# Performance work log

Hardware: AMD Instinct MI355X
Metric: run time of the kernel (lower is better)

## Reference

```python
import jax, jax.numpy as jnp
import numpy as np

K = 16  # neighbors


def _knn_indices(coords, k):
    # coords: (B, 3, N) -> indices (B, N, k) of k nearest points (incl. self)
    sq = jnp.sum(coords * coords, axis=1)                      # (B, N)
    d2 = sq[:, :, None] + sq[:, None, :] - 2.0 * jnp.einsum('bcn,bcm->bnm', coords, coords)
    _, idx = jax.lax.top_k(-d2, k)                             # smallest distances
    return idx


def _gather(points, idx):
    # points: (B, C, N), idx: (B, N, k) -> (B, C, N, k)
    return jax.vmap(lambda p, i: p[:, i])(points, idx)


def setup_inputs() -> dict:
    key = jax.random.key(0)
    ks = jax.random.split(key, 8)
    B, N, C_IN, C_OUT = 4, 8192, 64, 64
    s = 0.05
    return {
        'features': jax.random.normal(ks[0], (B, C_IN, N), dtype=jnp.float32),
        'coords': jax.random.normal(ks[1], (B, 3, N), dtype=jnp.float32),
        'w_lin': jax.random.normal(ks[2], (3 * C_OUT, C_IN), dtype=jnp.float32) * s,
        'w_theta1': jax.random.normal(ks[3], (C_OUT, 3), dtype=jnp.float32) * s,
        'w_theta2': jax.random.normal(ks[4], (C_OUT, C_OUT), dtype=jnp.float32) * s,
        'w_gamma1': jax.random.normal(ks[5], (C_OUT, C_OUT), dtype=jnp.float32) * s,
        'w_gamma2': jax.random.normal(ks[6], (C_OUT, C_OUT), dtype=jnp.float32) * s,
    }


def reference(features, coords, w_lin, w_theta1, w_theta2, w_gamma1, w_gamma2):
    # KNN (int indices, non-differentiable)
    idx = _knn_indices(coords, K)                              # (B, N, k)

    knn_coords = _gather(coords, idx)                          # (B, 3, N, k)
    rel = coords[:, :, :, None] - knn_coords                   # localize * -1
    delta = jnp.einsum('oc,bcnk->bonk', w_theta1, rel)
    delta = jax.nn.relu(jnp.einsum('oc,bcnk->bonk', w_theta2, delta))  # (B, Co, N, k)

    # input linear -> phi, psi, alpha
    feat3 = jnp.einsum('oc,bcn->bon', w_lin, features)         # (B, 3*Co, N)
    phi, psi, alpha = jnp.split(feat3, 3, axis=1)

    psi_g = _gather(psi, idx)                                  # (B, Co, N, k)
    inputs_gamma = phi[:, :, :, None] - psi_g + delta          # localize*-1 + delta
    g = jnp.einsum('oc,bcnk->bonk', w_gamma1, inputs_gamma)
    g = jax.nn.relu(jnp.einsum('oc,bcnk->bonk', w_gamma2, g))
    rho = jax.nn.softmax(g, axis=-1)                           # softmax over k

    alpha_g = _gather(alpha, idx) + delta                      # (B, Co, N, k)
    return jnp.sum(rho * alpha_g, axis=-1)                     # (B, Co, N)
```

## Files before the change

### kernel.cpp

```cpp
#include <hip/hip_runtime.h>
#include <cstdint>


#define NPT 8192
typedef unsigned long long u64;
typedef unsigned int u32;
typedef unsigned short u16;
typedef __attribute__((ext_vector_type(8))) short bf8_t;
typedef __attribute__((ext_vector_type(4))) float f32x4;

__device__ __forceinline__ u16 f2bf(float x) {
  return (u16)((__float_as_uint(x) + 0x8000u) >> 16);
}
__device__ __forceinline__ u32 pkbf(float lo, float hi) {
  return (u32)f2bf(lo) | ((u32)f2bf(hi) << 16);
}
__device__ __forceinline__ float bf2f(u16 v) {
  return __uint_as_float((u32)v << 16);
}
__device__ __forceinline__ u32 med3u(u32 a, u32 b, u32 c) {
  u32 d;
  asm("v_med3_u32 %0, %1, %2, %3" : "=v"(d) : "v"(a), "v"(b), "v"(c));
  return d;
}
__device__ __forceinline__ u32 wave_min_u32(u32 v) {
  u32 t;
  t = (u32)__builtin_amdgcn_update_dpp((int)v, (int)v, 0x111, 0xF, 0xF, false); v = min(v, t);
  t = (u32)__builtin_amdgcn_update_dpp((int)v, (int)v, 0x112, 0xF, 0xF, false); v = min(v, t);
  t = (u32)__builtin_amdgcn_update_dpp((int)v, (int)v, 0x114, 0xF, 0xF, false); v = min(v, t);
  t = (u32)__builtin_amdgcn_update_dpp((int)v, (int)v, 0x118, 0xF, 0xF, false); v = min(v, t);
  t = (u32)__builtin_amdgcn_update_dpp((int)v, (int)v, 0x142, 0xF, 0xF, false); v = min(v, t);
  t = (u32)__builtin_amdgcn_update_dpp((int)v, (int)v, 0x143, 0xF, 0xF, false); v = min(v, t);
  return (u32)__builtin_amdgcn_readlane((int)v, 63);
}

__global__ __launch_bounds__(256) void fold1_k(
    const float* __restrict__ wg1, const float* __restrict__ wg2,
    const float* __restrict__ wt1, const float* __restrict__ wt2,
    float* __restrict__ G, float* __restrict__ Mrow, float* __restrict__ McT) {
  int t = blockIdx.x * 256 + threadIdx.x;
  if (t < 4096) {
    int o = t >> 6, c = t & 63;
    float acc = 0.f;
    for (int cp = 0; cp < 64; ++cp) acc = fmaf(wg2[o * 64 + cp], wg1[cp * 64 + c], acc);
    G[o * 64 + c] = acc;
  } else if (t < 4096 + 192) {
    int i = t - 4096;
    int o = i / 3, j = i - o * 3;
    float acc = 0.f;
    for (int c = 0; c < 64; ++c) acc = fmaf(wt2[o * 64 + c], wt1[c * 3 + j], acc);
    Mrow[o * 3 + j] = acc;
    McT[j * 64 + o] = acc;
  }
}

__global__ __launch_bounds__(256) void fold2_k(
    const float* __restrict__ G, const float* __restrict__ wl,
    u16* __restrict__ GF, u16* __restrict__ WF) {
  int t = blockIdx.x * 256 + threadIdx.x;
  if (t < 12288) {
    int o = t >> 6, c = t & 63;
    float acc = 0.f;
    if (o < 64) {
      for (int cp = 0; cp < 64; ++cp) acc = fmaf(G[o * 64 + cp], wl[cp * 64 + c], acc);
    } else if (o < 128) {
      for (int cp = 0; cp < 64; ++cp) acc = fmaf(G[(o - 64) * 64 + cp], wl[(64 + cp) * 64 + c], acc);
    } else {
      acc = wl[o * 64 + c];
    }
    int ot = o >> 4, m = o & 15;
    int kh = c >> 5, q = (c >> 3) & 3, j = c & 7;
    WF[(((ot * 2 + kh) * 64) + (q * 16 + m)) * 8 + j] = f2bf(acc);
  } else {
    int i = t - 12288;
    int o = i >> 6, c = i & 63;
    int ot = o >> 4, m = o & 15;
    int kh = c >> 5, q = (c >> 3) & 3, j = c & 7;
    GF[(((ot * 2 + kh) * 64) + (q * 16 + m)) * 8 + j] = f2bf(G[o * 64 + c]);
  }
}

__global__ __launch_bounds__(256) void pack_k(const float* __restrict__ coords,
                                              float4* __restrict__ pack) {
  int g = blockIdx.x * 256 + threadIdx.x;
  int b = g >> 13, n = g & (NPT - 1);
  const float* c = coords + (size_t)b * 3 * NPT;
  float x = c[n], y = c[NPT + n], z = c[2 * NPT + n];
  float sq = __fadd_rn(__fadd_rn(__fmul_rn(x, x), __fmul_rn(y, y)), __fmul_rn(z, z));
  pack[g] = make_float4(x, y, z, sq);
}

#define QPB 8
#define CHUNK 1024
#define NQ 32768
__global__ __launch_bounds__(512) void knn_k(const float4* __restrict__ pack,
                                             u32* __restrict__ part, int qbase) {
  __shared__ float4 C[CHUNK];
  int tid = threadIdx.x;
  int w = tid >> 6, lane = tid & 63;
  int query = qbase + blockIdx.x * QPB + w;
  int b = query >> 13, n = query & (NPT - 1);
  const float4* pk = pack + (size_t)b * NPT;
  float4 q = pk[n];
  float qsq = q.w;
  u32 arr[8];
#pragma unroll
  for (int j = 0; j < 8; ++j) arr[j] = 0xFFFFFFFFu;
  for (int c0 = 0; c0 < NPT; c0 += CHUNK) {
    C[tid] = pk[c0 + tid];
    C[tid + 512] = pk[c0 + tid + 512];
    __syncthreads();
#pragma unroll 4
    for (int t = 0; t < CHUNK / 64; ++t) {
      float4 c4 = C[t * 64 + lane];
      float dot = fmaf(q.z, c4.z, fmaf(q.y, c4.y, q.x * c4.x));
      float d2 = fmaxf(fmaf(-2.f, dot, qsq + c4.w), 0.f);
      u32 key = (__float_as_uint(d2) & 0xFFFFE000u) | (u32)(c0 + t * 64 + lane);
      if (key < arr[7]) {
        arr[7] = med3u(key, arr[6], arr[7]);
        arr[6] = med3u(key, arr[5], arr[6]);
        arr[5] = med3u(key, arr[4], arr[5]);
        arr[4] = med3u(key, arr[3], arr[4]);
        arr[3] = med3u(key, arr[2], arr[3]);
        arr[2] = med3u(key, arr[1], arr[2]);
        arr[1] = med3u(key, arr[0], arr[1]);
        arr[0] = min(arr[0], key);
      }
    }
    __syncthreads();
  }
  u32 mg = 0xFFFFFFFFu;
#pragma unroll 1
  for (int r = 0; r < 24; ++r) {
    u32 m = wave_min_u32(arr[0]);
    if (lane == r) mg = m;
    if (arr[0] == m) {
      arr[0] = arr[1]; arr[1] = arr[2]; arr[2] = arr[3]; arr[3] = arr[4];
      arr[4] = arr[5]; arr[5] = arr[6]; arr[6] = arr[7]; arr[7] = 0xFFFFFFFFu;
    }
  }
  if (lane < 24) part[(size_t)lane * NQ + query] = mg;
}

__global__ __launch_bounds__(64) void refine_k(const float4* __restrict__ pack,
                                               const u32* __restrict__ part,
                                               int* __restrict__ idxk) {
  int g = blockIdx.x * 64 + threadIdx.x;
  int b = g >> 13;
  const float4* pk = pack + (size_t)b * NPT;
  float4 q = pk[g & (NPT - 1)];
  float qx = q.x, qy = q.y, qz = q.z, qs = q.w;
  float bd[16];
  int bi[16];
#pragma unroll
  for (int j = 0; j < 16; ++j) { bd[j] = 1e30f; bi[j] = 0x7FFFFFFF; }
#pragma unroll 4
  for (int j = 0; j < 24; ++j) {
    int m = (int)(part[(size_t)j * NQ + g] & 0x1FFFu);
    float4 pm = pk[m];
    float dot = __fadd_rn(__fadd_rn(__fmul_rn(qx, pm.x), __fmul_rn(qy, pm.y)),
                          __fmul_rn(qz, pm.z));
    float kd = __fsub_rn(__fadd_rn(qs, pm.w), __fmul_rn(2.0f, dot));
    int ki = m;
    if (kd < bd[15] || (kd == bd[15] && ki < bi[15])) {
#pragma unroll
      for (int qq = 0; qq < 16; ++qq) {
        bool cs = (kd < bd[qq]) || (kd == bd[qq] && ki < bi[qq]);
        float td = bd[qq];
        int ti = bi[qq];
        bd[qq] = cs ? kd : td;
        bi[qq] = cs ? ki : ti;
        kd = cs ? td : kd;
        ki = cs ? ti : ki;
      }
    }
  }
#pragma unroll
  for (int j = 0; j < 16; ++j) idxk[(size_t)g * 16 + j] = bi[j];
}

__global__ __launch_bounds__(256) void feat_k(const float* __restrict__ features,
                                              const u16* __restrict__ WF,
                                              float* __restrict__ featA,
                                              u16* __restrict__ featB) {
  int tid = threadIdx.x;
  int w = tid >> 6, l = tid & 63;
  int quad = l >> 4, col = l & 15;
  int P = blockIdx.x * 64 + w * 16 + col;
  int b = P >> 13, n = P & (NPT - 1);
  const float* fb = features + (size_t)b * 64 * NPT + n;
  const bf8_t* wfr = (const bf8_t*)WF;
  bf8_t Bf[2];
#pragma unroll
  for (int kh = 0; kh < 2; ++kh) {
    union { u32 wv[4]; bf8_t v; } ub;
#pragma unroll
    for (int j2 = 0; j2 < 4; ++j2) {
      float lo = fb[(size_t)(kh * 32 + quad * 8 + j2 * 2) * NPT];
      float hi = fb[(size_t)(kh * 32 + quad * 8 + j2 * 2 + 1) * NPT];
      ub.wv[j2] = pkbf(lo, hi);
    }
    Bf[kh] = ub.v;
  }
#pragma unroll
  for (int ot = 0; ot < 12; ++ot) {
    bf8_t A0 = wfr[(ot * 2 + 0) * 64 + l];
    bf8_t A1 = wfr[(ot * 2 + 1) * 64 + l];
    f32x4 acc = {0.f, 0.f, 0.f, 0.f};
    acc = __builtin_amdgcn_mfma_f32_16x16x32_bf16(A0, Bf[0], acc, 0, 0, 0);
    acc = __builtin_amdgcn_mfma_f32_16x16x32_bf16(A1, Bf[1], acc, 0, 0, 0);
    int gr = ot * 16 + quad * 4;
    if (ot < 4) {
      *(float4*)(featA + (size_t)P * 64 + gr) = make_float4(acc[0], acc[1], acc[2], acc[3]);
    } else {
      uint2 wv2 = make_uint2(pkbf(acc[0], acc[1]), pkbf(acc[2], acc[3]));
      *(uint2*)(featB + (size_t)P * 128 + (gr - 64)) = wv2;
    }
  }
}

#define SROW 68
__global__ __launch_bounds__(64) void attn_k(
    const float4* __restrict__ pack, const int* __restrict__ idxk,
    const float* __restrict__ featA, const u16* __restrict__ featB,
    const u16* __restrict__ GF, const float* __restrict__ Mrow,
    const float* __restrict__ McT, float* __restrict__ out) {
  __shared__ u16 S16[64 * SROW];
  int l = threadIdx.x;
  int quad = l >> 4, col = l & 15;
  int Pb = blockIdx.x * 4;
  int b = Pb >> 13;
  int nb0 = Pb & (NPT - 1);
  const float4* pkb = pack + (size_t)b * NPT;
  int idxv = idxk[(size_t)Pb * 16 + l];
  int mve[4];
#pragma unroll
  for (int t = 0; t < 4; ++t) mve[t] = __shfl(idxv, t * 16 + col);
  float relx[4], rely[4], relz[4];
#pragma unroll
  for (int t = 0; t < 4; ++t) {
    float4 own = pkb[nb0 + t];
    float4 nbr = pkb[mve[t]];
    relx[t] = own.x - nbr.x; rely[t] = own.y - nbr.y; relz[t] = own.z - nbr.z;
  }
  bf8_t Bf[4][2];
#pragma unroll
  for (int kh = 0; kh < 2; ++kh) {
    const float* mr = Mrow + (kh * 32 + quad * 8) * 3;
    float m_[24];
#pragma unroll
    for (int i6 = 0; i6 < 6; ++i6) {
      float4 v = *(const float4*)(mr + i6 * 4);
      m_[i6 * 4] = v.x; m_[i6 * 4 + 1] = v.y; m_[i6 * 4 + 2] = v.z; m_[i6 * 4 + 3] = v.w;
    }
#pragma unroll
    for (int t = 0; t < 4; ++t) {
      float u_[8];
#pragma unroll
      for (int j = 0; j < 8; ++j)
        u_[j] = fmaxf(fmaf(m_[j * 3 + 2], relz[t],
                           fmaf(m_[j * 3 + 1], rely[t], m_[j * 3] * relx[t])), 0.f);
      union { u32 w[4]; bf8_t v; } ub;
#pragma unroll
      for (int j2 = 0; j2 < 4; ++j2) ub.w[j2] = pkbf(u_[j2 * 2], u_[j2 * 2 + 1]);
      Bf[t][kh] = ub.v;
    }
  }
  const bf8_t* gfr = (const bf8_t*)GF;
#pragma unroll
  for (int ot = 0; ot < 4; ++ot) {
    bf8_t A0 = gfr[(ot * 2 + 0) * 64 + l];
    bf8_t A1 = gfr[(ot * 2 + 1) * 64 + l];
#pragma unroll
    for (int pt = 0; pt < 4; ++pt) {
      f32x4 acc = {0.f, 0.f, 0.f, 0.f};
      acc = __builtin_amdgcn_mfma_f32_16x16x32_bf16(A0, Bf[pt][0], acc, 0, 0, 0);
      acc = __builtin_amdgcn_mfma_f32_16x16x32_bf16(A1, Bf[pt][1], acc, 0, 0, 0);
      const float* phn = featA + (size_t)(Pb + pt) * 64 + ot * 16 + quad * 4;
      float4 ph = *(const float4*)phn;
      uint2 psw = *(const uint2*)(featB + ((size_t)b * NPT + mve[pt]) * 128 + ot * 16 + quad * 4);
      float g0 = fmaxf(acc[0] + ph.x - bf2f((u16)(psw.x & 0xFFFF)), 0.f);
      float g1 = fmaxf(acc[1] + ph.y - bf2f((u16)(psw.x >> 16)), 0.f);
      float g2 = fmaxf(acc[2] + ph.z - bf2f((u16)(psw.y & 0xFFFF)), 0.f);
      float g3 = fmaxf(acc[3] + ph.w - bf2f((u16)(psw.y >> 16)), 0.f);
      uint2 wv = make_uint2(pkbf(g0, g1), pkbf(g2, g3));
      *(uint2*)&S16[(pt * 16 + col) * SROW + ot * 16 + quad * 4] = wv;
    }
  }
  __syncthreads();
  float mc0 = McT[l], mc1 = McT[64 + l], mc2 = McT[128 + l];
  float accv[4];
#pragma unroll 1
  for (int pj = 0; pj < 4; ++pj) {
    float4 ownq = pkb[nb0 + pj];
    float gvv[16];
    float mx = -1e30f;
#pragma unroll
    for (int r = 0; r < 16; ++r) {
      gvv[r] = bf2f(S16[(pj * 16 + r) * SROW + l]);
      mx = fmaxf(mx, gvv[r]);
    }
    float s = 0.f;
#pragma unroll
    for (int r = 0; r < 16; ++r) {
      float e = __expf(gvv[r] - mx);
      gvv[r] = e;
      s += e;
    }
    float inv = 1.0f / s;
    float acc = 0.f;
#pragma unroll
    for (int r = 0; r < 16; ++r) {
      int si = __builtin_amdgcn_readlane(idxv, pj * 16 + r);
      float4 nbq = pkb[si];
      float dl = fmaxf(fmaf(mc2, ownq.z - nbq.z,
                            fmaf(mc1, ownq.y - nbq.y, mc0 * (ownq.x - nbq.x))), 0.f);
      float al = bf2f(featB[((size_t)b * NPT + si) * 128 + 64 + l]);
      acc = fmaf(gvv[r] * inv, al + dl, acc);
    }
    accv[pj] = acc;
  }
  *(float4*)(out + ((size_t)b * 64 + l) * NPT + nb0) =
      make_float4(accv[0], accv[1], accv[2], accv[3]);
}

extern "C" void kernel_launch(void* const* d_in, const int* in_sizes, int n_in,
                              void* d_out, int out_size, void* d_ws, size_t ws_size,
                              hipStream_t stream) {
  const float* features = (const float*)d_in[0];
  const float* coords = (const float*)d_in[1];
  const float* w_lin = (const float*)d_in[2];
  const float* w_t1 = (const float*)d_in[3];
  const float* w_t2 = (const float*)d_in[4];
  const float* w_g1 = (const float*)d_in[5];
  const float* w_g2 = (const float*)d_in[6];
  float* out = (float*)d_out;
  char* ws = (char*)d_ws;
  float4* pack = (float4*)ws;
  float* G = (float*)(ws + 524288);
  float* Mrow = (float*)(ws + 540672);
  float* McT = (float*)(ws + 541440);
  int* idxk = (int*)(ws + 591360);
  float* featA = (float*)(ws + 2688512);
  u16* featB = (u16*)(ws + 11077120);
  u32* part = (u32*)(ws + 2688512);
  u16* GF = (u16*)(ws + 19465728);
  u16* WF = (u16*)(ws + 19473920);

  fold1_k<<<17, 256, 0, stream>>>(w_g1, w_g2, w_t1, w_t2, G, Mrow, McT);
  fold2_k<<<64, 256, 0, stream>>>(G, w_lin, GF, WF);
  pack_k<<<128, 256, 0, stream>>>(coords, pack);
  knn_k<<<1024, 512, 0, stream>>>(pack, part, 0);
  knn_k<<<1024, 512, 0, stream>>>(pack, part, 8192);
  knn_k<<<1024, 512, 0, stream>>>(pack, part, 16384);
  knn_k<<<1024, 512, 0, stream>>>(pack, part, 24576);
  refine_k<<<512, 64, 0, stream>>>(pack, part, idxk);
  feat_k<<<512, 256, 0, stream>>>(features, WF, featA, featB);
  attn_k<<<8192, 64, 0, stream>>>(pack, idxk, featA, featB, GF, Mrow, McT, out);
}
```

Before: 307.2 us.

## Double-buffer KNN candidate chunks with async LDS loads and prune by wave threshold

The KNN kernel now stages candidate chunks into a double-buffered LDS array using global_load_lds. The next chunk is prefetched while the current one is scanned, and the barrier before the scan is dropped. After each chunk it computes a wave-wide threshold: the maximum over lanes of each lane's best key. Later candidates above that threshold skip the sorted-insert sequence, which is safe because at least 64 better keys already exist. The four per-batch launches are merged into one grid of 4096 blocks. This doubles LDS use per block, which may reduce occupancy, and correctness depends on the async copies finishing before the barrier.

```diff
diff --git a/kernel.cpp b/kernel.cpp
--- a/kernel.cpp
+++ b/kernel.cpp
@@ -32,6 +32,21 @@
   t = (u32)__builtin_amdgcn_update_dpp((int)v, (int)v, 0x142, 0xF, 0xF, false); v = min(v, t);
   t = (u32)__builtin_amdgcn_update_dpp((int)v, (int)v, 0x143, 0xF, 0xF, false); v = min(v, t);
   return (u32)__builtin_amdgcn_readlane((int)v, 63);
+}
+__device__ __forceinline__ u32 wave_max_u32(u32 v) {
+  u32 t;
+  t = (u32)__builtin_amdgcn_update_dpp((int)v, (int)v, 0x111, 0xF, 0xF, false); v = max(v, t);
+  t = (u32)__builtin_amdgcn_update_dpp((int)v, (int)v, 0x112, 0xF, 0xF, false); v = max(v, t);
+  t = (u32)__builtin_amdgcn_update_dpp((int)v, (int)v, 0x114, 0xF, 0xF, false); v = max(v, t);
+  t = (u32)__builtin_amdgcn_update_dpp((int)v, (int)v, 0x118, 0xF, 0xF, false); v = max(v, t);
+  t = (u32)__builtin_amdgcn_update_dpp((int)v, (int)v, 0x142, 0xF, 0xF, false); v = max(v, t);
+  t = (u32)__builtin_amdgcn_update_dpp((int)v, (int)v, 0x143, 0xF, 0xF, false); v = max(v, t);
+  return (u32)__builtin_amdgcn_readlane((int)v, 63);
+}
+__device__ __forceinline__ void lds_cp16(float4* lds_dst, const float4* gsrc) {
+  __builtin_amdgcn_global_load_lds(
+      (const __attribute__((address_space(1))) unsigned int*)(const void*)gsrc,
+      (__attribute__((address_space(3))) unsigned int*)(void*)lds_dst, 16, 0, 0);
 }
 
 __global__ __launch_bounds__(256) void fold1_k(
@@ -94,11 +109,11 @@
 #define CHUNK 1024
 #define NQ 32768
 __global__ __launch_bounds__(512) void knn_k(const float4* __restrict__ pack,
-                                             u32* __restrict__ part, int qbase) {
-  __shared__ float4 C[CHUNK];
+                                             u32* __restrict__ part) {
+  __shared__ float4 C[2][CHUNK];
   int tid = threadIdx.x;
   int w = tid >> 6, lane = tid & 63;
-  int query = qbase + blockIdx.x * QPB + w;
+  int query = blockIdx.x * QPB + w;
   int b = query >> 13, n = query & (NPT - 1);
   const float4* pk = pack + (size_t)b * NPT;
   float4 q = pk[n];
@@ -106,17 +121,23 @@
   u32 arr[8];
 #pragma unroll
   for (int j = 0; j < 8; ++j) arr[j] = 0xFFFFFFFFu;
+  lds_cp16(&C[0][tid], pk + tid);
+  lds_cp16(&C[0][512 + tid], pk + 512 + tid);
+  __syncthreads();
+  u32 tau = 0xFFFFFFFFu;
   for (int c0 = 0; c0 < NPT; c0 += CHUNK) {
-    C[tid] = pk[c0 + tid];
-    C[tid + 512] = pk[c0 + tid + 512];
-    __syncthreads();
+    int cur = (c0 >> 10) & 1;
+    if (c0 + CHUNK < NPT) {
+      lds_cp16(&C[cur ^ 1][tid], pk + (c0 + CHUNK) + tid);
+      lds_cp16(&C[cur ^ 1][512 + tid], pk + (c0 + CHUNK) + 512 + tid);
+    }
 #pragma unroll 4
     for (int t = 0; t < CHUNK / 64; ++t) {
-      float4 c4 = C[t * 64 + lane];
+      float4 c4 = C[cur][t * 64 + lane];
       float dot = fmaf(q.z, c4.z, fmaf(q.y, c4.y, q.x * c4.x));
       float d2 = fmaxf(fmaf(-2.f, dot, qsq + c4.w), 0.f);
       u32 key = (__float_as_uint(d2) & 0xFFFFE000u) | (u32)(c0 + t * 64 + lane);
-      if (key < arr[7]) {
+      if (key < min(arr[7], tau)) {
         arr[7] = med3u(key, arr[6], arr[7]);
         arr[6] = med3u(key, arr[5], arr[6]);
         arr[5] = med3u(key, arr[4], arr[5]);
@@ -127,6 +148,7 @@
         arr[0] = min(arr[0], key);
       }
     }
+    tau = wave_max_u32(arr[0]);
     __syncthreads();
   }
   u32 mg = 0xFFFFFFFFu;
@@ -350,10 +372,7 @@
   fold1_k<<<17, 256, 0, stream>>>(w_g1, w_g2, w_t1, w_t2, G, Mrow, McT);
   fold2_k<<<64, 256, 0, stream>>>(G, w_lin, GF, WF);
   pack_k<<<128, 256, 0, stream>>>(coords, pack);
-  knn_k<<<1024, 512, 0, stream>>>(pack, part, 0);
-  knn_k<<<1024, 512, 0, stream>>>(pack, part, 8192);
-  knn_k<<<1024, 512, 0, stream>>>(pack, part, 16384);
-  knn_k<<<1024, 512, 0, stream>>>(pack, part, 24576);
+  knn_k<<<4096, 512, 0, stream>>>(pack, part);
   refine_k<<<512, 64, 0, stream>>>(pack, part, idxk);
   feat_k<<<512, 256, 0, stream>>>(features, WF, featA, featB);
   attn_k<<<8192, 64, 0, stream>>>(pack, idxk, featA, featB, GF, Mrow, McT, out);
```

Measured after the change: 294.2 us. -4.2%, faster.
